# Performance work log

Hardware: AMD Instinct MI355X
Metric: run time of the kernel (lower is better)

The kernel has to match this reference:

```python
import jax, jax.numpy as jnp
import numpy as np

DIM = 512
DIM_HEAD = 64
HEADS = 8
SCALE = 8.0  # Attend(scale=8)
DIM_INNER = DIM_HEAD * HEADS


def setup_inputs() -> dict:
    key = jax.random.key(0)
    k1, k2, k3, k4 = jax.random.split(key, 4)
    b, n = 8, 4096
    x = jax.random.normal(k1, (b, n, DIM), dtype=jnp.float32)
    gamma = jnp.ones((DIM,), dtype=jnp.float32)
    w_qkv = jax.random.normal(k2, (DIM, 3 * DIM_INNER), dtype=jnp.float32) * (DIM ** -0.5)
    temperature = jnp.ones((HEADS, 1, 1), dtype=jnp.float32)
    w_out = jax.random.normal(k3, (DIM_INNER, DIM), dtype=jnp.float32) * (DIM_INNER ** -0.5)
    return {"x": x, "gamma": gamma, "w_qkv": w_qkv, "temperature": temperature, "w_out": w_out}


def _l2norm(t, axis=-1, eps=1e-12):
    return t / jnp.maximum(jnp.linalg.norm(t, axis=axis, keepdims=True), eps)


def reference(x, gamma, w_qkv, temperature, w_out):
    b, n, _ = x.shape
    # RMSNorm: F.normalize(x, dim=-1) * sqrt(dim) * gamma
    xn = _l2norm(x) * (DIM ** 0.5) * gamma
    qkv = xn @ w_qkv                                   # [b, n, 3*h*d]
    qkv = qkv.reshape(b, n, 3, HEADS, DIM_HEAD)
    qkv = jnp.transpose(qkv, (2, 0, 3, 4, 1))          # [3, b, h, d, n]
    q, k, v = qkv[0], qkv[1], qkv[2]
    q = _l2norm(q)                                     # l2norm over n (last dim)
    k = _l2norm(k)
    q = q * jnp.exp(temperature)                       # [h,1,1] broadcast
    sim = jnp.einsum('bhdn,bhen->bhde', q, k) * SCALE  # [b, h, d, d]
    attn = jax.nn.softmax(sim, axis=-1)
    out = jnp.einsum('bhde,bhen->bhdn', attn, v)       # [b, h, d, n]
    out = jnp.transpose(out, (0, 3, 1, 2)).reshape(b, n, DIM_INNER)
    return out @ w_out
```

## Files before the change

kernel.cpp:

```cpp
#include <hip/hip_runtime.h>
#include <stdint.h>

#define NDIM 512
#define HEADS 8
#define DHEAD 64
#define NSEQ 4096
#define BATCH 8
#define ROWS (BATCH * NSEQ)
#define QKVN (3 * NDIM)

typedef unsigned short ushort_t;
typedef __bf16 bf16x8 __attribute__((ext_vector_type(8)));
typedef float f32x4 __attribute__((ext_vector_type(4)));
typedef unsigned short u16x8 __attribute__((ext_vector_type(8)));
typedef unsigned short u16x4 __attribute__((ext_vector_type(4)));

__device__ __forceinline__ ushort_t f2bf(float f) {
  union { float f; uint32_t u; } v; v.f = f;
  uint32_t r = (v.u + 0x7FFFu + ((v.u >> 16) & 1u)) >> 16;
  return (ushort_t)r;
}
__device__ __forceinline__ float bf2f(ushort_t h) {
  union { uint32_t u; float f; } v; v.u = ((uint32_t)h) << 16;
  return v.f;
}

__device__ __forceinline__ void gload_lds16(const void* g, void* l) {
  __builtin_amdgcn_global_load_lds(
      (__attribute__((address_space(1))) void*)(g),
      (__attribute__((address_space(3))) void*)(l), 16, 0, 0);
}

__global__ __launch_bounds__(256) void prep_k(const float* __restrict__ w_qkv,
                                              const float* __restrict__ w_out,
                                              ushort_t* __restrict__ wqkvT,
                                              ushort_t* __restrict__ woutT) {
  __shared__ float tile[32][33];
  int id = blockIdx.x;
  const float* src;
  ushort_t* dst;
  int srcStride, ni, ki;
  if (id < 768) {
    ni = id % 48; ki = id / 48; src = w_qkv; dst = wqkvT; srcStride = QKVN;
  } else {
    id -= 768;
    ni = id % 16; ki = id / 16; src = w_out; dst = woutT; srcStride = NDIM;
  }
  int tr = threadIdx.x >> 3;
  int tc = (threadIdx.x & 7) * 4;
  float4 v = *(const float4*)(src + (size_t)(ki * 32 + tr) * srcStride + ni * 32 + tc);
  tile[tr][tc] = v.x; tile[tr][tc + 1] = v.y; tile[tr][tc + 2] = v.z; tile[tr][tc + 3] = v.w;
  __syncthreads();
  u16x4 o;
  o[0] = f2bf(tile[tc + 0][tr]);
  o[1] = f2bf(tile[tc + 1][tr]);
  o[2] = f2bf(tile[tc + 2][tr]);
  o[3] = f2bf(tile[tc + 3][tr]);
  *(u16x4*)(dst + (size_t)(ni * 32 + tr) * NDIM + ki * 32 + tc) = o;
}

__global__ __launch_bounds__(256) void rmsnorm_k(const float* __restrict__ x,
                                                 const float* __restrict__ gamma,
                                                 ushort_t* __restrict__ xn) {
  int wave = threadIdx.x >> 6, lane = threadIdx.x & 63;
  size_t row = (size_t)blockIdx.x * 4 + wave;
  const float4* xr = (const float4*)(x + row * NDIM);
  float4 v0 = xr[lane * 2], v1 = xr[lane * 2 + 1];
  float s = v0.x*v0.x + v0.y*v0.y + v0.z*v0.z + v0.w*v0.w
          + v1.x*v1.x + v1.y*v1.y + v1.z*v1.z + v1.w*v1.w;
#pragma unroll
  for (int off = 32; off; off >>= 1) s += __shfl_xor(s, off, 64);
  float scale = 22.627416997969522f / fmaxf(sqrtf(s), 1e-12f);
  const float4* gr = (const float4*)gamma;
  float4 g0 = gr[lane * 2], g1 = gr[lane * 2 + 1];
  u16x8 o;
  o[0] = f2bf(v0.x * scale * g0.x);
  o[1] = f2bf(v0.y * scale * g0.y);
  o[2] = f2bf(v0.z * scale * g0.z);
  o[3] = f2bf(v0.w * scale * g0.w);
  o[4] = f2bf(v1.x * scale * g1.x);
  o[5] = f2bf(v1.y * scale * g1.y);
  o[6] = f2bf(v1.z * scale * g1.z);
  o[7] = f2bf(v1.w * scale * g1.w);
  *(u16x8*)(xn + row * NDIM + lane * 8) = o;
}

template <bool OUT_BF16>
__device__ __forceinline__ void gemm256x128_core(
    const ushort_t* __restrict__ A, size_t strideA, size_t m0,
    const ushort_t* __restrict__ B,
    void* __restrict__ C, size_t strideC, size_t n0,
    ushort_t* sm) {
  const int tid  = threadIdx.x;
  const int lane = tid & 63;
  const int wave = tid >> 6;
  const int srow = lane >> 3;
  const int scol = ((lane & 7) ^ srow) * 16;
  const int r = lane & 15, q = lane >> 4;
  const int wm = (wave >> 1) * 64;
  const int wn = (wave & 1) * 64;

  ushort_t* As = sm;
  ushort_t* Bs = sm + 49152;

  auto stageA = [&](int t2, int g) {
    gload_lds16((const char*)(A + (m0 + (size_t)(g * 8 + srow)) * strideA + t2 * 64) + scol,
                (char*)(As + (t2 % 3) * 16384 + g * 512));
  };
  auto stageB = [&](int t2, int g) {
    gload_lds16((const char*)(B + (size_t)(g * 8 + srow) * NDIM + t2 * 64) + scol,
                (char*)(Bs + (t2 % 3) * 8192 + g * 512));
  };

#pragma unroll
  for (int t2 = 0; t2 < 2; ++t2) {
#pragma unroll
    for (int a = 0; a < 4; ++a) stageA(t2, wave * 4 + a);
#pragma unroll
    for (int bb = 0; bb < 2; ++bb) stageB(t2, wave * 2 + bb);
  }
  asm volatile("s_waitcnt vmcnt(6)" ::: "memory");
  __builtin_amdgcn_s_barrier();

  f32x4 acc[4][4] = {};

#pragma unroll
  for (int t = 0; t < 8; ++t) {
    const ushort_t* Ab = As + (t % 3) * 16384;
    const ushort_t* Bb = Bs + (t % 3) * 8192;
#pragma unroll
    for (int ph = 0; ph < 2; ++ph) {
      const int kb = ph * 4 + q;
      bf16x8 af[4], bfr[4];
#pragma unroll
      for (int i = 0; i < 4; ++i) {
        int row = wm + i * 16 + r;
        af[i] = *(const bf16x8*)(const void*)(Ab + row * 64 + ((kb ^ (row & 7)) << 3));
      }
#pragma unroll
      for (int j = 0; j < 4; ++j) {
        int row = wn + j * 16 + r;
        bfr[j] = *(const bf16x8*)(const void*)(Bb + row * 64 + ((kb ^ (row & 7)) << 3));
      }
      if (t < 6) {
        int t2 = t + 2;
        if (ph == 0) { stageA(t2, wave * 4 + 0); stageA(t2, wave * 4 + 1); stageB(t2, wave * 2 + 0); }
        else         { stageA(t2, wave * 4 + 2); stageA(t2, wave * 4 + 3); stageB(t2, wave * 2 + 1); }
      }
      __builtin_amdgcn_s_barrier();
      asm volatile("s_waitcnt lgkmcnt(0)" ::: "memory");
      __builtin_amdgcn_s_setprio(1);
#pragma unroll
      for (int i = 0; i < 4; ++i)
#pragma unroll
        for (int j = 0; j < 4; ++j)
          acc[i][j] = __builtin_amdgcn_mfma_f32_16x16x32_bf16(af[i], bfr[j], acc[i][j], 0, 0, 0);
      __builtin_amdgcn_s_setprio(0);
      if (ph == 1) {
        if (t < 6)       { asm volatile("s_waitcnt vmcnt(6)" ::: "memory"); }
        else if (t == 6) { asm volatile("s_waitcnt vmcnt(0)" ::: "memory"); }
      }
      __builtin_amdgcn_s_barrier();
    }
  }

  __syncthreads();
  if constexpr (OUT_BF16) {
    ushort_t* Cb = sm;
    ushort_t* Cc = (ushort_t*)C;
#pragma unroll
    for (int i = 0; i < 4; ++i)
#pragma unroll
      for (int j = 0; j < 4; ++j)
#pragma unroll
        for (int v = 0; v < 4; ++v)
          Cb[(wm + i * 16 + q * 4 + v) * 136 + wn + j * 16 + r] = f2bf(acc[i][j][v]);
    __syncthreads();
#pragma unroll
    for (int it = 0; it < 8; ++it) {
      int row = (tid >> 4) + it * 32;
      int col = (tid & 15) * 8;
      u16x8 val = *(const u16x8*)(Cb + row * 136 + col);
      *(u16x8*)(Cc + (m0 + row) * strideC + n0 + col) = val;
    }
  } else {
    float* Cf = (float*)sm;
    float* Co = (float*)C;
#pragma unroll
    for (int p = 0; p < 2; ++p) {
      __syncthreads();
      if (((wave >> 2) & 1) == p) {
#pragma unroll
        for (int i = 0; i < 4; ++i)
#pragma unroll
          for (int j = 0; j < 4; ++j)
#pragma unroll
            for (int v = 0; v < 4; ++v)
              Cf[((wm & 127) + i * 16 + q * 4 + v) * 132 + wn + j * 16 + r] = acc[i][j][v];
      }
      __syncthreads();
      int row = tid >> 2;
      int c0 = (tid & 3) * 4;
#pragma unroll
      for (int it = 0; it < 8; ++it) {
        int col = c0 + it * 16;
        f32x4 val = *(const f32x4*)(Cf + row * 132 + col);
        *(f32x4*)(Co + (m0 + p * 128 + row) * strideC + n0 + col) = val;
      }
    }
  }
}

__global__ __launch_bounds__(512, 2) void gemm_qkv(const ushort_t* __restrict__ A,
                                                   const ushort_t* __restrict__ BT,
                                                   ushort_t* __restrict__ C) {
  __shared__ __align__(16) ushort_t sm[73728];
  const int flat = blockIdx.x;
  const int xcd = flat & 7;
  const int idx = flat >> 3;
  const int local_m = idx / 12;
  const int n_t = idx - local_m * 12;
  const size_t m0 = (size_t)(xcd * 16 + local_m) * 256;
  const size_t n0 = (size_t)n_t * 128;
  gemm256x128_core<true>(A, NDIM, m0, BT + n0 * NDIM, C, QKVN, n0, sm);
}

__global__ __launch_bounds__(256) void gram_k(const ushort_t* __restrict__ qkv,
                                              float* __restrict__ pG,
                                              float* __restrict__ pSq) {
  int chunk = blockIdx.x;
  int bh = blockIdx.y;
  int b = bh >> 3, h = bh & 7;
  __shared__ ushort_t Qt[64 * 72];
  __shared__ ushort_t Kt[64 * 72];
  __shared__ float sq[128];
  int tid = threadIdx.x, lane = tid & 63, wave = tid >> 6;
  int nl = tid >> 2;
  int dp = (tid & 3) * 16;
  int r = lane & 15, q = lane >> 4;
  float aq[16] = {}, ak[16] = {};
  f32x4 acc[4] = {};
  size_t base_row = ((size_t)b * NSEQ + (size_t)chunk * 512) * QKVN + (size_t)h * DHEAD;
  int swz_n = ((nl >> 3) & 7);
  int c_lo = (nl & 7) | (((swz_n ^ (dp >> 3)) & 7) << 3);
  int c_hi = (nl & 7) | (((swz_n ^ ((dp >> 3) + 1)) & 7) << 3);
  ushort_t* qlo = Qt + dp * 72 + c_lo;
  ushort_t* qhi = Qt + (dp + 8) * 72 + c_hi;
  ushort_t* klo = Kt + dp * 72 + c_lo;
  ushort_t* khi = Kt + (dp + 8) * 72 + c_hi;

  for (int sc = 0; sc < 8; ++sc) {
    __syncthreads();
    size_t g = base_row + (size_t)(sc * 64 + nl) * QKVN;
    u16x8 qv0 = *(const u16x8*)(qkv + g + dp);
    u16x8 qv1 = *(const u16x8*)(qkv + g + dp + 8);
    u16x8 kv0 = *(const u16x8*)(qkv + g + NDIM + dp);
    u16x8 kv1 = *(const u16x8*)(qkv + g + NDIM + dp + 8);
#pragma unroll
    for (int i = 0; i < 8; ++i) {
      float fq = bf2f(qv0[i]); aq[i] += fq * fq;       qlo[i * 72] = qv0[i];
      float fq2 = bf2f(qv1[i]); aq[8 + i] += fq2 * fq2; qhi[i * 72] = qv1[i];
      float fk = bf2f(kv0[i]); ak[i] += fk * fk;       klo[i * 72] = kv0[i];
      float fk2 = bf2f(kv1[i]); ak[8 + i] += fk2 * fk2; khi[i * 72] = kv1[i];
    }
    __syncthreads();
#pragma unroll
    for (int ks = 0; ks < 64; ks += 32) {
      int kb = (ks >> 3) + q;
      int m = wave * 16 + r;
      bf16x8 a = *(const bf16x8*)(const void*)(Qt + m * 72 + (((kb ^ (m >> 3)) & 7) << 3));
#pragma unroll
      for (int j = 0; j < 4; ++j) {
        int e = j * 16 + r;
        bf16x8 bb = *(const bf16x8*)(const void*)(Kt + e * 72 + (((kb ^ (e >> 3)) & 7) << 3));
        acc[j] = __builtin_amdgcn_mfma_f32_16x16x32_bf16(a, bb, acc[j], 0, 0, 0);
      }
    }
  }
  size_t gbase = ((size_t)bh * 8 + chunk) * 4096;
#pragma unroll
  for (int j = 0; j < 4; ++j)
#pragma unroll
    for (int v = 0; v < 4; ++v)
      pG[gbase + (size_t)(wave * 16 + q * 4 + v) * 64 + j * 16 + r] = acc[j][v];
  if (tid < 128) sq[tid] = 0.f;
  __syncthreads();
#pragma unroll
  for (int i = 0; i < 16; ++i) {
    atomicAdd(&sq[dp + i], aq[i]);
    atomicAdd(&sq[64 + dp + i], ak[i]);
  }
  __syncthreads();
  if (tid < 128) pSq[((size_t)bh * 8 + chunk) * 128 + tid] = sq[tid];
}

__global__ __launch_bounds__(256) void softmax_k(const float* __restrict__ pG,
                                                 const float* __restrict__ pSq,
                                                 const float* __restrict__ temp,
                                                 ushort_t* __restrict__ attnT) {
  int bh = blockIdx.x;
  int h = bh & 7;
  int t = threadIdx.x;
  int d = t >> 2;
  int eg = (t & 3) * 16;
  __shared__ float kn[64];
  if (t < 64) {
    float sk = 0.f;
    for (int c = 0; c < 8; ++c) sk += pSq[((size_t)bh * 8 + c) * 128 + 64 + t];
    kn[t] = fmaxf(sqrtf(sk), 1e-12f);
  }
  float sq = 0.f;
  for (int c = 0; c < 8; ++c) sq += pSq[((size_t)bh * 8 + c) * 128 + d];
  float qn = fmaxf(sqrtf(sq), 1e-12f);
  __syncthreads();
  float scale = 8.0f * expf(temp[h]) / qn;
  float row[16];
#pragma unroll
  for (int k = 0; k < 16; ++k) row[k] = 0.f;
  for (int c = 0; c < 8; ++c) {
    const float4* src = (const float4*)(pG + ((size_t)bh * 8 + c) * 4096 + d * 64 + eg);
#pragma unroll
    for (int k4 = 0; k4 < 4; ++k4) {
      float4 v = src[k4];
      row[k4 * 4 + 0] += v.x; row[k4 * 4 + 1] += v.y;
      row[k4 * 4 + 2] += v.z; row[k4 * 4 + 3] += v.w;
    }
  }
#pragma unroll
  for (int k = 0; k < 16; ++k) row[k] = row[k] * scale / kn[eg + k];
  float mx = -1e30f;
#pragma unroll
  for (int k = 0; k < 16; ++k) mx = fmaxf(mx, row[k]);
  mx = fmaxf(mx, __shfl_xor(mx, 1, 64));
  mx = fmaxf(mx, __shfl_xor(mx, 2, 64));
  float s = 0.f;
#pragma unroll
  for (int k = 0; k < 16; ++k) { row[k] = expf(row[k] - mx); s += row[k]; }
  s += __shfl_xor(s, 1, 64);
  s += __shfl_xor(s, 2, 64);
  float inv = 1.0f / s;
#pragma unroll
  for (int k = 0; k < 16; ++k)
    attnT[(size_t)bh * 4096 + (eg + k) * 64 + d] = f2bf(row[k] * inv);
}

__global__ __launch_bounds__(256) void w2t_k(const ushort_t* __restrict__ woutT,
                                             const ushort_t* __restrict__ attnT,
                                             ushort_t* __restrict__ W2T) {
  int mq = blockIdx.x;
  int bh = blockIdx.y;
  int b = bh >> 3, h = bh & 7;
  int tid = threadIdx.x, lane = tid & 63, wave = tid >> 6;
  int r = lane & 15, q = lane >> 4;
  int mbase = mq * 128 + wave * 32;
  const ushort_t* At = attnT + (size_t)bh * 4096;
  f32x4 acc[2][4] = {};
#pragma unroll
  for (int kk = 0; kk < 64; kk += 32) {
    bf16x8 a[2], bb[4];
#pragma unroll
    for (int mf = 0; mf < 2; ++mf)
      a[mf] = *(const bf16x8*)(woutT + (size_t)(mbase + mf * 16 + r) * NDIM + h * 64 + kk + q * 8);
#pragma unroll
    for (int nf = 0; nf < 4; ++nf)
      bb[nf] = *(const bf16x8*)(At + (nf * 16 + r) * 64 + kk + q * 8);
#pragma unroll
    for (int mf = 0; mf < 2; ++mf)
#pragma unroll
      for (int nf = 0; nf < 4; ++nf)
        acc[mf][nf] = __builtin_amdgcn_mfma_f32_16x16x32_bf16(a[mf], bb[nf], acc[mf][nf], 0, 0, 0);
  }
#pragma unroll
  for (int mf = 0; mf < 2; ++mf)
#pragma unroll
    for (int nf = 0; nf < 4; ++nf)
#pragma unroll
      for (int v = 0; v < 4; ++v)
        W2T[(size_t)b * 262144 + (size_t)(mbase + mf * 16 + q * 4 + v) * NDIM +
            h * 64 + nf * 16 + r] = f2bf(acc[mf][nf][v]);
}

__global__ __launch_bounds__(512, 2) void gemm_v(const ushort_t* __restrict__ qkv,
                                                 const ushort_t* __restrict__ W2T,
                                                 float* __restrict__ out) {
  __shared__ __align__(16) ushort_t sm[73728];
  const int flat = blockIdx.x;
  const int b = flat & 7;
  const int local = flat >> 3;
  const int mt = local >> 2, nt = local & 3;
  const size_t m0 = (size_t)b * NSEQ + (size_t)mt * 256;
  const size_t n0 = (size_t)nt * 128;
  gemm256x128_core<false>(qkv + 1024, QKVN, m0,
                          W2T + (size_t)b * 262144 + n0 * NDIM,
                          out, NDIM, n0, sm);
}

extern "C" void kernel_launch(void* const* d_in, const int* in_sizes, int n_in,
                              void* d_out, int out_size, void* d_ws, size_t ws_size,
                              hipStream_t stream) {
  (void)in_sizes; (void)n_in; (void)out_size; (void)ws_size;
  const float* x     = (const float*)d_in[0];
  const float* gamma = (const float*)d_in[1];
  const float* w_qkv = (const float*)d_in[2];
  const float* temp  = (const float*)d_in[3];
  const float* w_out = (const float*)d_in[4];
  float* out = (float*)d_out;
  char* ws = (char*)d_ws;

  ushort_t* qkv   = (ushort_t*)ws;
  ushort_t* xn    = (ushort_t*)(ws + (size_t)100663296);
  float*    pG    = (float*)(ws + (size_t)100663296);
  float*    pSq   = (float*)(ws + (size_t)100663296 + 8388608);
  ushort_t* W2T   = (ushort_t*)(ws + (size_t)100663296 + 12582912);
  ushort_t* wqkvT = (ushort_t*)(ws + (size_t)134217728);
  ushort_t* woutT = (ushort_t*)(ws + (size_t)134217728 + 1572864);
  ushort_t* attnT = (ushort_t*)(ws + (size_t)134217728 + 2097152);

  prep_k<<<1024, 256, 0, stream>>>(w_qkv, w_out, wqkvT, woutT);
  rmsnorm_k<<<ROWS / 4, 256, 0, stream>>>(x, gamma, xn);
  gemm_qkv<<<(QKVN / 128) * (ROWS / 256), 512, 0, stream>>>(xn, wqkvT, qkv);
  gram_k<<<dim3(8, 64), 256, 0, stream>>>(qkv, pG, pSq);
  softmax_k<<<64, 256, 0, stream>>>(pG, pSq, temp, attnT);
  w2t_k<<<dim3(4, 64), 256, 0, stream>>>(woutT, attnT, W2T);
  gemm_v<<<(NDIM / 128) * (ROWS / 256), 512, 0, stream>>>(qkv, W2T, out);
}
```

Before: 260.2 us.

## Enlarge GEMM tiles to 256x256 with a three-slot K pipeline

The shared GEMM core now computes 256x256 output tiles instead of 256x128, with each wave holding an 8x4 MFMA accumulator block. K is staged in 32-wide slices across three LDS buffers in a fragment-contiguous layout that replaces the XOR swizzle. The epilogues are reworked to write in halves or quarters. This halves the block count and raises arithmetic intensity per loaded byte, at the cost of doubled accumulator registers, 96KB of LDS per block (which may cut occupancy from two blocks per CU), and a risk of LDS bank conflicts without the swizzle.

```diff
diff --git a/kernel.cpp b/kernel.cpp
--- a/kernel.cpp
+++ b/kernel.cpp
@@ -86,126 +86,117 @@
 }
 
 template <bool OUT_BF16>
-__device__ __forceinline__ void gemm256x128_core(
-    const ushort_t* __restrict__ A, size_t strideA, size_t m0,
-    const ushort_t* __restrict__ B,
-    void* __restrict__ C, size_t strideC, size_t n0,
-    ushort_t* sm) {
+__device__ __forceinline__ void gemm256core(
+    const ushort_t* __restrict__ A, int strideA,
+    const ushort_t* __restrict__ B, int strideB,
+    void* __restrict__ C, int strideC, size_t crow0, int n0,
+    char* sm) {
   const int tid  = threadIdx.x;
   const int lane = tid & 63;
   const int wave = tid >> 6;
-  const int srow = lane >> 3;
-  const int scol = ((lane & 7) ^ srow) * 16;
-  const int r = lane & 15, q = lane >> 4;
-  const int wm = (wave >> 1) * 64;
-  const int wn = (wave & 1) * 64;
-
-  ushort_t* As = sm;
-  ushort_t* Bs = sm + 49152;
-
-  auto stageA = [&](int t2, int g) {
-    gload_lds16((const char*)(A + (m0 + (size_t)(g * 8 + srow)) * strideA + t2 * 64) + scol,
-                (char*)(As + (t2 % 3) * 16384 + g * 512));
+  const int r = lane & 15;
+  const int q = lane >> 4;
+  const int wmg = (wave >> 2) * 8;
+  const int wng = (wave & 3) * 4;
+
+  char* As = sm;
+  char* Bs = sm + 49152;
+
+  auto stage = [&](int h) {
+    const int slot = h % 3;
+    const int colu = h * 32 + q * 8;
+#pragma unroll
+    for (int u = 0; u < 2; ++u) {
+      const int g = wave * 2 + u;
+      gload_lds16(A + (size_t)(g * 16 + r) * strideA + colu,
+                  As + slot * 16384 + g * 1024);
+      gload_lds16(B + (size_t)(g * 16 + r) * strideB + colu,
+                  Bs + slot * 16384 + g * 1024);
+    }
   };
-  auto stageB = [&](int t2, int g) {
-    gload_lds16((const char*)(B + (size_t)(g * 8 + srow) * NDIM + t2 * 64) + scol,
-                (char*)(Bs + (t2 % 3) * 8192 + g * 512));
-  };
-
-#pragma unroll
-  for (int t2 = 0; t2 < 2; ++t2) {
-#pragma unroll
-    for (int a = 0; a < 4; ++a) stageA(t2, wave * 4 + a);
-#pragma unroll
-    for (int bb = 0; bb < 2; ++bb) stageB(t2, wave * 2 + bb);
-  }
-  asm volatile("s_waitcnt vmcnt(6)" ::: "memory");
+
+#pragma unroll
+  for (int h = 0; h < 3; ++h) stage(h);
+  asm volatile("s_waitcnt vmcnt(8)" ::: "memory");
   __builtin_amdgcn_s_barrier();
 
-  f32x4 acc[4][4] = {};
-
-#pragma unroll
-  for (int t = 0; t < 8; ++t) {
-    const ushort_t* Ab = As + (t % 3) * 16384;
-    const ushort_t* Bb = Bs + (t % 3) * 8192;
-#pragma unroll
-    for (int ph = 0; ph < 2; ++ph) {
-      const int kb = ph * 4 + q;
-      bf16x8 af[4], bfr[4];
-#pragma unroll
-      for (int i = 0; i < 4; ++i) {
-        int row = wm + i * 16 + r;
-        af[i] = *(const bf16x8*)(const void*)(Ab + row * 64 + ((kb ^ (row & 7)) << 3));
+  f32x4 acc[8][4] = {};
+
+#pragma unroll
+  for (int h = 0; h < 16; ++h) {
+    const char* Ah = As + (h % 3) * 16384;
+    const char* Bh = Bs + (h % 3) * 16384;
+    bf16x8 af[8], bfr[4];
+#pragma unroll
+    for (int i = 0; i < 8; ++i)
+      af[i] = *(const bf16x8*)(Ah + (wmg + i) * 1024 + q * 256 + r * 16);
+#pragma unroll
+    for (int j = 0; j < 4; ++j)
+      bfr[j] = *(const bf16x8*)(Bh + (wng + j) * 1024 + q * 256 + r * 16);
+    if (h >= 1 && h <= 13) stage(h + 2);
+    asm volatile("s_waitcnt lgkmcnt(0)" ::: "memory");
+    __builtin_amdgcn_sched_barrier(0);
+    __builtin_amdgcn_s_setprio(1);
+#pragma unroll
+    for (int i = 0; i < 8; ++i)
+#pragma unroll
+      for (int j = 0; j < 4; ++j)
+        acc[i][j] = __builtin_amdgcn_mfma_f32_16x16x32_bf16(af[i], bfr[j], acc[i][j], 0, 0, 0);
+    __builtin_amdgcn_s_setprio(0);
+    if (h <= 13)      { asm volatile("s_waitcnt vmcnt(4)" ::: "memory"); }
+    else if (h == 14) { asm volatile("s_waitcnt vmcnt(0)" ::: "memory"); }
+    __builtin_amdgcn_s_barrier();
+  }
+
+  if constexpr (OUT_BF16) {
+    ushort_t* Cb = (ushort_t*)sm;
+    ushort_t* Cc = (ushort_t*)C;
+#pragma unroll
+    for (int p = 0; p < 2; ++p) {
+      __syncthreads();
+      if ((wave >> 2) == p) {
+#pragma unroll
+        for (int i = 0; i < 8; ++i)
+#pragma unroll
+          for (int j = 0; j < 4; ++j)
+#pragma unroll
+            for (int v = 0; v < 4; ++v)
+              Cb[(i * 16 + q * 4 + v) * 264 + (wave & 3) * 64 + j * 16 + r] =
+                  f2bf(acc[i][j][v]);
       }
-#pragma unroll
-      for (int j = 0; j < 4; ++j) {
-        int row = wn + j * 16 + r;
-        bfr[j] = *(const bf16x8*)(const void*)(Bb + row * 64 + ((kb ^ (row & 7)) << 3));
+      __syncthreads();
+#pragma unroll
+      for (int it = 0; it < 8; ++it) {
+        int row = (tid >> 5) + it * 16;
+        int ch = tid & 31;
+        u16x8 val = *(const u16x8*)(Cb + row * 264 + ch * 8);
+        *(u16x8*)(Cc + (crow0 + p * 128 + row) * strideC + n0 + ch * 8) = val;
       }
-      if (t < 6) {
-        int t2 = t + 2;
-        if (ph == 0) { stageA(t2, wave * 4 + 0); stageA(t2, wave * 4 + 1); stageB(t2, wave * 2 + 0); }
-        else         { stageA(t2, wave * 4 + 2); stageA(t2, wave * 4 + 3); stageB(t2, wave * 2 + 1); }
-      }
-      __builtin_amdgcn_s_barrier();
-      asm volatile("s_waitcnt lgkmcnt(0)" ::: "memory");
-      __builtin_amdgcn_s_setprio(1);
-#pragma unroll
-      for (int i = 0; i < 4; ++i)
-#pragma unroll
-        for (int j = 0; j < 4; ++j)
-          acc[i][j] = __builtin_amdgcn_mfma_f32_16x16x32_bf16(af[i], bfr[j], acc[i][j], 0, 0, 0);
-      __builtin_amdgcn_s_setprio(0);
-      if (ph == 1) {
-        if (t < 6)       { asm volatile("s_waitcnt vmcnt(6)" ::: "memory"); }
-        else if (t == 6) { asm volatile("s_waitcnt vmcnt(0)" ::: "memory"); }
-      }
-      __builtin_amdgcn_s_barrier();
-    }
-  }
-
-  __syncthreads();
-  if constexpr (OUT_BF16) {
-    ushort_t* Cb = sm;
-    ushort_t* Cc = (ushort_t*)C;
-#pragma unroll
-    for (int i = 0; i < 4; ++i)
-#pragma unroll
-      for (int j = 0; j < 4; ++j)
-#pragma unroll
-        for (int v = 0; v < 4; ++v)
-          Cb[(wm + i * 16 + q * 4 + v) * 136 + wn + j * 16 + r] = f2bf(acc[i][j][v]);
-    __syncthreads();
-#pragma unroll
-    for (int it = 0; it < 8; ++it) {
-      int row = (tid >> 4) + it * 32;
-      int col = (tid & 15) * 8;
-      u16x8 val = *(const u16x8*)(Cb + row * 136 + col);
-      *(u16x8*)(Cc + (m0 + row) * strideC + n0 + col) = val;
     }
   } else {
     float* Cf = (float*)sm;
     float* Co = (float*)C;
 #pragma unroll
-    for (int p = 0; p < 2; ++p) {
+    for (int p = 0; p < 4; ++p) {
       __syncthreads();
-      if (((wave >> 2) & 1) == p) {
-#pragma unroll
-        for (int i = 0; i < 4; ++i)
+      if ((wave >> 2) == (p >> 1)) {
+        const int ib = (p & 1) * 4;
+#pragma unroll
+        for (int i2 = 0; i2 < 4; ++i2)
 #pragma unroll
           for (int j = 0; j < 4; ++j)
 #pragma unroll
             for (int v = 0; v < 4; ++v)
-              Cf[((wm & 127) + i * 16 + q * 4 + v) * 132 + wn + j * 16 + r] = acc[i][j][v];
+              Cf[(i2 * 16 + q * 4 + v) * 260 + (wave & 3) * 64 + j * 16 + r] =
+                  acc[ib + i2][j][v];
       }
       __syncthreads();
-      int row = tid >> 2;
-      int c0 = (tid & 3) * 4;
 #pragma unroll
       for (int it = 0; it < 8; ++it) {
-        int col = c0 + it * 16;
-        f32x4 val = *(const f32x4*)(Cf + row * 132 + col);
-        *(f32x4*)(Co + (m0 + p * 128 + row) * strideC + n0 + col) = val;
+        int row = (tid >> 6) + it * 8;
+        int c4 = (tid & 63) * 4;
+        f32x4 val = *(const f32x4*)(Cf + row * 260 + c4);
+        *(f32x4*)(Co + (crow0 + p * 64 + row) * strideC + n0 + c4) = val;
       }
     }
   }
@@ -214,15 +205,17 @@
 __global__ __launch_bounds__(512, 2) void gemm_qkv(const ushort_t* __restrict__ A,
                                                    const ushort_t* __restrict__ BT,
                                                    ushort_t* __restrict__ C) {
-  __shared__ __align__(16) ushort_t sm[73728];
+  __shared__ __align__(16) char sm[98304];
   const int flat = blockIdx.x;
   const int xcd = flat & 7;
-  const int idx = flat >> 3;
-  const int local_m = idx / 12;
-  const int n_t = idx - local_m * 12;
-  const size_t m0 = (size_t)(xcd * 16 + local_m) * 256;
-  const size_t n0 = (size_t)n_t * 128;
-  gemm256x128_core<true>(A, NDIM, m0, BT + n0 * NDIM, C, QKVN, n0, sm);
+  const int local = flat >> 3;
+  const int lm = local / 6;
+  const int nt = local - lm * 6;
+  const size_t m0 = (size_t)(xcd * 16 + lm) * 256;
+  const int n0 = nt * 256;
+  gemm256core<true>(A + m0 * NDIM, NDIM,
+                    BT + (size_t)n0 * NDIM, NDIM,
+                    C, QKVN, m0, n0, sm);
 }
 
 __global__ __launch_bounds__(256) void gram_k(const ushort_t* __restrict__ qkv,
@@ -383,16 +376,16 @@
 __global__ __launch_bounds__(512, 2) void gemm_v(const ushort_t* __restrict__ qkv,
                                                  const ushort_t* __restrict__ W2T,
                                                  float* __restrict__ out) {
-  __shared__ __align__(16) ushort_t sm[73728];
+  __shared__ __align__(16) char sm[98304];
   const int flat = blockIdx.x;
   const int b = flat & 7;
   const int local = flat >> 3;
-  const int mt = local >> 2, nt = local & 3;
+  const int mt = local >> 1, nt = local & 1;
   const size_t m0 = (size_t)b * NSEQ + (size_t)mt * 256;
-  const size_t n0 = (size_t)nt * 128;
-  gemm256x128_core<false>(qkv + 1024, QKVN, m0,
-                          W2T + (size_t)b * 262144 + n0 * NDIM,
-                          out, NDIM, n0, sm);
+  const int n0 = nt * 256;
+  gemm256core<false>(qkv + m0 * QKVN + 1024, QKVN,
+                     W2T + (size_t)b * 262144 + (size_t)n0 * NDIM, NDIM,
+                     out, NDIM, m0, n0, sm);
 }
 
 extern "C" void kernel_launch(void* const* d_in, const int* in_sizes, int n_in,
@@ -418,9 +411,9 @@
 
   prep_k<<<1024, 256, 0, stream>>>(w_qkv, w_out, wqkvT, woutT);
   rmsnorm_k<<<ROWS / 4, 256, 0, stream>>>(x, gamma, xn);
-  gemm_qkv<<<(QKVN / 128) * (ROWS / 256), 512, 0, stream>>>(xn, wqkvT, qkv);
+  gemm_qkv<<<(QKVN / 256) * (ROWS / 256), 512, 0, stream>>>(xn, wqkvT, qkv);
   gram_k<<<dim3(8, 64), 256, 0, stream>>>(qkv, pG, pSq);
   softmax_k<<<64, 256, 0, stream>>>(pG, pSq, temp, attnT);
   w2t_k<<<dim3(4, 64), 256, 0, stream>>>(woutT, attnT, W2T);
-  gemm_v<<<(NDIM / 128) * (ROWS / 256), 512, 0, stream>>>(qkv, W2T, out);
-}
+  gemm_v<<<(NDIM / 256) * (ROWS / 256), 512, 0, stream>>>(qkv, W2T, out);
+}
```

Result: no change. 262.7 us (+0.9%).

## Fuse weight prep with RMSNorm and softmax with attn-by-Wout product

Applied to the files above, without the earlier changes.

Weight transpose/convert and RMSNorm now run in one launch by splitting on block index, and the softmax kernel is merged into the W2T kernel. The attention matrix stays in XOR-swizzled shared memory instead of making a global round trip. Each of the 4 blocks per head recomputes the same softmax, so that small work is done four times to save two launches and one global buffer. The bf16 epilogue store also has its addressing rewritten in bytes, which does not change the computation.

```diff
diff --git a/kernel.cpp b/kernel.cpp
--- a/kernel.cpp
+++ b/kernel.cpp
@@ -31,58 +31,59 @@
       (__attribute__((address_space(3))) void*)(l), 16, 0, 0);
 }
 
-__global__ __launch_bounds__(256) void prep_k(const float* __restrict__ w_qkv,
-                                              const float* __restrict__ w_out,
-                                              ushort_t* __restrict__ wqkvT,
-                                              ushort_t* __restrict__ woutT) {
+__global__ __launch_bounds__(256) void prep_rms_k(const float* __restrict__ x,
+                                                  const float* __restrict__ gamma,
+                                                  ushort_t* __restrict__ xn,
+                                                  const float* __restrict__ w_qkv,
+                                                  const float* __restrict__ w_out,
+                                                  ushort_t* __restrict__ wqkvT,
+                                                  ushort_t* __restrict__ woutT) {
   __shared__ float tile[32][33];
-  int id = blockIdx.x;
-  const float* src;
-  ushort_t* dst;
-  int srcStride, ni, ki;
-  if (id < 768) {
-    ni = id % 48; ki = id / 48; src = w_qkv; dst = wqkvT; srcStride = QKVN;
+  if (blockIdx.x < 8192) {
+    int wave = threadIdx.x >> 6, lane = threadIdx.x & 63;
+    size_t row = (size_t)blockIdx.x * 4 + wave;
+    const float4* xr = (const float4*)(x + row * NDIM);
+    float4 v0 = xr[lane * 2], v1 = xr[lane * 2 + 1];
+    float s = v0.x*v0.x + v0.y*v0.y + v0.z*v0.z + v0.w*v0.w
+            + v1.x*v1.x + v1.y*v1.y + v1.z*v1.z + v1.w*v1.w;
+#pragma unroll
+    for (int off = 32; off; off >>= 1) s += __shfl_xor(s, off, 64);
+    float scale = 22.627416997969522f / fmaxf(sqrtf(s), 1e-12f);
+    const float4* gr = (const float4*)gamma;
+    float4 g0 = gr[lane * 2], g1 = gr[lane * 2 + 1];
+    u16x8 o;
+    o[0] = f2bf(v0.x * scale * g0.x);
+    o[1] = f2bf(v0.y * scale * g0.y);
+    o[2] = f2bf(v0.z * scale * g0.z);
+    o[3] = f2bf(v0.w * scale * g0.w);
+    o[4] = f2bf(v1.x * scale * g1.x);
+    o[5] = f2bf(v1.y * scale * g1.y);
+    o[6] = f2bf(v1.z * scale * g1.z);
+    o[7] = f2bf(v1.w * scale * g1.w);
+    *(u16x8*)(xn + row * NDIM + lane * 8) = o;
   } else {
-    id -= 768;
-    ni = id % 16; ki = id / 16; src = w_out; dst = woutT; srcStride = NDIM;
-  }
-  int tr = threadIdx.x >> 3;
-  int tc = (threadIdx.x & 7) * 4;
-  float4 v = *(const float4*)(src + (size_t)(ki * 32 + tr) * srcStride + ni * 32 + tc);
-  tile[tr][tc] = v.x; tile[tr][tc + 1] = v.y; tile[tr][tc + 2] = v.z; tile[tr][tc + 3] = v.w;
-  __syncthreads();
-  u16x4 o;
-  o[0] = f2bf(tile[tc + 0][tr]);
-  o[1] = f2bf(tile[tc + 1][tr]);
-  o[2] = f2bf(tile[tc + 2][tr]);
-  o[3] = f2bf(tile[tc + 3][tr]);
-  *(u16x4*)(dst + (size_t)(ni * 32 + tr) * NDIM + ki * 32 + tc) = o;
-}
-
-__global__ __launch_bounds__(256) void rmsnorm_k(const float* __restrict__ x,
-                                                 const float* __restrict__ gamma,
-                                                 ushort_t* __restrict__ xn) {
-  int wave = threadIdx.x >> 6, lane = threadIdx.x & 63;
-  size_t row = (size_t)blockIdx.x * 4 + wave;
-  const float4* xr = (const float4*)(x + row * NDIM);
-  float4 v0 = xr[lane * 2], v1 = xr[lane * 2 + 1];
-  float s = v0.x*v0.x + v0.y*v0.y + v0.z*v0.z + v0.w*v0.w
-          + v1.x*v1.x + v1.y*v1.y + v1.z*v1.z + v1.w*v1.w;
-#pragma unroll
-  for (int off = 32; off; off >>= 1) s += __shfl_xor(s, off, 64);
-  float scale = 22.627416997969522f / fmaxf(sqrtf(s), 1e-12f);
-  const float4* gr = (const float4*)gamma;
-  float4 g0 = gr[lane * 2], g1 = gr[lane * 2 + 1];
-  u16x8 o;
-  o[0] = f2bf(v0.x * scale * g0.x);
-  o[1] = f2bf(v0.y * scale * g0.y);
-  o[2] = f2bf(v0.z * scale * g0.z);
-  o[3] = f2bf(v0.w * scale * g0.w);
-  o[4] = f2bf(v1.x * scale * g1.x);
-  o[5] = f2bf(v1.y * scale * g1.y);
-  o[6] = f2bf(v1.z * scale * g1.z);
-  o[7] = f2bf(v1.w * scale * g1.w);
-  *(u16x8*)(xn + row * NDIM + lane * 8) = o;
+    int id = blockIdx.x - 8192;
+    const float* src;
+    ushort_t* dst;
+    int srcStride, ni, ki;
+    if (id < 768) {
+      ni = id % 48; ki = id / 48; src = w_qkv; dst = wqkvT; srcStride = QKVN;
+    } else {
+      id -= 768;
+      ni = id % 16; ki = id / 16; src = w_out; dst = woutT; srcStride = NDIM;
+    }
+    int tr = threadIdx.x >> 3;
+    int tc = (threadIdx.x & 7) * 4;
+    float4 v = *(const float4*)(src + (size_t)(ki * 32 + tr) * srcStride + ni * 32 + tc);
+    tile[tr][tc] = v.x; tile[tr][tc + 1] = v.y; tile[tr][tc + 2] = v.z; tile[tr][tc + 3] = v.w;
+    __syncthreads();
+    u16x4 o;
+    o[0] = f2bf(tile[tc + 0][tr]);
+    o[1] = f2bf(tile[tc + 1][tr]);
+    o[2] = f2bf(tile[tc + 2][tr]);
+    o[3] = f2bf(tile[tc + 3][tr]);
+    *(u16x4*)(dst + (size_t)(ni * 32 + tr) * NDIM + ki * 32 + tc) = o;
+  }
 }
 
 template <bool OUT_BF16>
@@ -179,10 +180,11 @@
 #pragma unroll
     for (int it = 0; it < 8; ++it) {
       int row = (tid >> 4) + it * 32;
-      int col = (tid & 15) * 8;
-      u16x8 val = *(const u16x8*)(Cb + row * 136 + col);
-      *(u16x8*)(Cc + (m0 + row) * strideC + n0 + col) = val;
-    }
+      int colB = (tid & 15) * 16;
+      u16x8 val = *(const u16x8*)((const char*)Cb + row * 272 + colB);
+      *(u16x8*)((char*)((ushort_t*)C + (m0 + row) * strideC + n0) + colB) = val;
+    }
+    (void)Cc;
   } else {
     float* Cf = (float*)sm;
     float* Co = (float*)C;
@@ -294,66 +296,67 @@
   if (tid < 128) pSq[((size_t)bh * 8 + chunk) * 128 + tid] = sq[tid];
 }
 
-__global__ __launch_bounds__(256) void softmax_k(const float* __restrict__ pG,
-                                                 const float* __restrict__ pSq,
-                                                 const float* __restrict__ temp,
-                                                 ushort_t* __restrict__ attnT) {
-  int bh = blockIdx.x;
-  int h = bh & 7;
-  int t = threadIdx.x;
-  int d = t >> 2;
-  int eg = (t & 3) * 16;
-  __shared__ float kn[64];
-  if (t < 64) {
-    float sk = 0.f;
-    for (int c = 0; c < 8; ++c) sk += pSq[((size_t)bh * 8 + c) * 128 + 64 + t];
-    kn[t] = fmaxf(sqrtf(sk), 1e-12f);
-  }
-  float sq = 0.f;
-  for (int c = 0; c < 8; ++c) sq += pSq[((size_t)bh * 8 + c) * 128 + d];
-  float qn = fmaxf(sqrtf(sq), 1e-12f);
-  __syncthreads();
-  float scale = 8.0f * expf(temp[h]) / qn;
-  float row[16];
-#pragma unroll
-  for (int k = 0; k < 16; ++k) row[k] = 0.f;
-  for (int c = 0; c < 8; ++c) {
-    const float4* src = (const float4*)(pG + ((size_t)bh * 8 + c) * 4096 + d * 64 + eg);
-#pragma unroll
-    for (int k4 = 0; k4 < 4; ++k4) {
-      float4 v = src[k4];
-      row[k4 * 4 + 0] += v.x; row[k4 * 4 + 1] += v.y;
-      row[k4 * 4 + 2] += v.z; row[k4 * 4 + 3] += v.w;
-    }
-  }
-#pragma unroll
-  for (int k = 0; k < 16; ++k) row[k] = row[k] * scale / kn[eg + k];
-  float mx = -1e30f;
-#pragma unroll
-  for (int k = 0; k < 16; ++k) mx = fmaxf(mx, row[k]);
-  mx = fmaxf(mx, __shfl_xor(mx, 1, 64));
-  mx = fmaxf(mx, __shfl_xor(mx, 2, 64));
-  float s = 0.f;
-#pragma unroll
-  for (int k = 0; k < 16; ++k) { row[k] = expf(row[k] - mx); s += row[k]; }
-  s += __shfl_xor(s, 1, 64);
-  s += __shfl_xor(s, 2, 64);
-  float inv = 1.0f / s;
-#pragma unroll
-  for (int k = 0; k < 16; ++k)
-    attnT[(size_t)bh * 4096 + (eg + k) * 64 + d] = f2bf(row[k] * inv);
-}
-
-__global__ __launch_bounds__(256) void w2t_k(const ushort_t* __restrict__ woutT,
-                                             const ushort_t* __restrict__ attnT,
-                                             ushort_t* __restrict__ W2T) {
+__global__ __launch_bounds__(256) void smax_w2t_k(const float* __restrict__ pG,
+                                                  const float* __restrict__ pSq,
+                                                  const float* __restrict__ temp,
+                                                  const ushort_t* __restrict__ woutT,
+                                                  ushort_t* __restrict__ W2T) {
   int mq = blockIdx.x;
   int bh = blockIdx.y;
   int b = bh >> 3, h = bh & 7;
-  int tid = threadIdx.x, lane = tid & 63, wave = tid >> 6;
+  __shared__ ushort_t at[64 * 64];
+  __shared__ float kn[64];
+  int t = threadIdx.x;
+
+  {
+    int d = t >> 2;
+    int eg = (t & 3) * 16;
+    if (t < 64) {
+      float sk = 0.f;
+      for (int c = 0; c < 8; ++c) sk += pSq[((size_t)bh * 8 + c) * 128 + 64 + t];
+      kn[t] = fmaxf(sqrtf(sk), 1e-12f);
+    }
+    float sq = 0.f;
+    for (int c = 0; c < 8; ++c) sq += pSq[((size_t)bh * 8 + c) * 128 + d];
+    float qn = fmaxf(sqrtf(sq), 1e-12f);
+    __syncthreads();
+    float scale = 8.0f * expf(temp[h]) / qn;
+    float row[16];
+#pragma unroll
+    for (int k = 0; k < 16; ++k) row[k] = 0.f;
+    for (int c = 0; c < 8; ++c) {
+      const float4* src = (const float4*)(pG + ((size_t)bh * 8 + c) * 4096 + d * 64 + eg);
+#pragma unroll
+      for (int k4 = 0; k4 < 4; ++k4) {
+        float4 v = src[k4];
+        row[k4 * 4 + 0] += v.x; row[k4 * 4 + 1] += v.y;
+        row[k4 * 4 + 2] += v.z; row[k4 * 4 + 3] += v.w;
+      }
+    }
+#pragma unroll
+    for (int k = 0; k < 16; ++k) row[k] = row[k] * scale / kn[eg + k];
+    float mx = -1e30f;
+#pragma unroll
+    for (int k = 0; k < 16; ++k) mx = fmaxf(mx, row[k]);
+    mx = fmaxf(mx, __shfl_xor(mx, 1, 64));
+    mx = fmaxf(mx, __shfl_xor(mx, 2, 64));
+    float s = 0.f;
+#pragma unroll
+    for (int k = 0; k < 16; ++k) { row[k] = expf(row[k] - mx); s += row[k]; }
+    s += __shfl_xor(s, 1, 64);
+    s += __shfl_xor(s, 2, 64);
+    float inv = 1.0f / s;
+#pragma unroll
+    for (int k = 0; k < 16; ++k) {
+      int e = eg + k;
+      at[e * 64 + ((d & 7) | ((((d >> 3) ^ e) & 7) << 3))] = f2bf(row[k] * inv);
+    }
+  }
+  __syncthreads();
+
+  int lane = t & 63, wave = t >> 6;
   int r = lane & 15, q = lane >> 4;
   int mbase = mq * 128 + wave * 32;
-  const ushort_t* At = attnT + (size_t)bh * 4096;
   f32x4 acc[2][4] = {};
 #pragma unroll
   for (int kk = 0; kk < 64; kk += 32) {
@@ -362,8 +365,11 @@
     for (int mf = 0; mf < 2; ++mf)
       a[mf] = *(const bf16x8*)(woutT + (size_t)(mbase + mf * 16 + r) * NDIM + h * 64 + kk + q * 8);
 #pragma unroll
-    for (int nf = 0; nf < 4; ++nf)
-      bb[nf] = *(const bf16x8*)(At + (nf * 16 + r) * 64 + kk + q * 8);
+    for (int nf = 0; nf < 4; ++nf) {
+      int e = nf * 16 + r;
+      int c = (kk >> 3) + q;
+      bb[nf] = *(const bf16x8*)(const void*)(at + e * 64 + (((c ^ e) & 7) << 3));
+    }
 #pragma unroll
     for (int mf = 0; mf < 2; ++mf)
 #pragma unroll
@@ -414,13 +420,10 @@
   ushort_t* W2T   = (ushort_t*)(ws + (size_t)100663296 + 12582912);
   ushort_t* wqkvT = (ushort_t*)(ws + (size_t)134217728);
   ushort_t* woutT = (ushort_t*)(ws + (size_t)134217728 + 1572864);
-  ushort_t* attnT = (ushort_t*)(ws + (size_t)134217728 + 2097152);
-
-  prep_k<<<1024, 256, 0, stream>>>(w_qkv, w_out, wqkvT, woutT);
-  rmsnorm_k<<<ROWS / 4, 256, 0, stream>>>(x, gamma, xn);
+
+  prep_rms_k<<<ROWS / 4 + 1024, 256, 0, stream>>>(x, gamma, xn, w_qkv, w_out, wqkvT, woutT);
   gemm_qkv<<<(QKVN / 128) * (ROWS / 256), 512, 0, stream>>>(xn, wqkvT, qkv);
   gram_k<<<dim3(8, 64), 256, 0, stream>>>(qkv, pG, pSq);
-  softmax_k<<<64, 256, 0, stream>>>(pG, pSq, temp, attnT);
-  w2t_k<<<dim3(4, 64), 256, 0, stream>>>(woutT, attnT, W2T);
+  smax_w2t_k<<<dim3(4, 64), 256, 0, stream>>>(pG, pSq, temp, woutT, W2T);
   gemm_v<<<(NDIM / 128) * (ROWS / 256), 512, 0, stream>>>(qkv, W2T, out);
 }
```

Measured after the change: 261.0 us. About the same (+0.3%).
